# Performance work log

Hardware: AMD Instinct MI355X
Metric: run time of the kernel (lower is better)

The kernel has to match this reference:

```python
import jax, jax.numpy as jnp
import numpy as np

B, S = 2, 1024
ENC_IN, MARK_IN = 21, 4
PRED_LEN, C_OUT = 96, 21
E = 512                 # embedding_dim
INNER = 2 * E           # proj_factor=2.0 (library default; Model does not pass it)
NH = 8                  # mLSTM heads
DH = INNER // NH        # 128
K = 4                   # causal conv1d kernel
BS = 4                  # qkv_proj_blocksize
NHP = INNER // BS       # 256 block-diagonal proj heads
NB = 4                  # num_blocks
EPS = 1e-5


def setup_inputs() -> dict:
    key = jax.random.key(0)
    ks = jax.random.split(key, 24)
    it = iter(range(24))
    def n(shape, s=0.02):
        return jax.random.normal(ks[next(it)], shape, jnp.float32) * s
    return {
        "x_enc": n((B, S, ENC_IN), 1.0),
        "x_mark_enc": n((B, S, MARK_IN), 1.0),
        "x_dec": n((B, PRED_LEN, ENC_IN), 1.0),
        "x_mark_dec": n((B, PRED_LEN, MARK_IN), 1.0),
        "emb_W": n((ENC_IN + MARK_IN, E), 0.05),
        "emb_b": jnp.zeros((E,), jnp.float32),
        "ln_w": jnp.ones((NB, E), jnp.float32),
        "up_W": n((NB, E, 2 * INNER)),
        "conv_W": n((NB, INNER, K), 0.1),
        "conv_b": jnp.zeros((NB, INNER), jnp.float32),
        "q_W": n((NB, NHP, BS, BS), 0.1),
        "k_W": n((NB, NHP, BS, BS), 0.1),
        "v_W": n((NB, NHP, BS, BS), 0.1),
        "ig_W": n((NB, 3 * INNER, NH)),
        "ig_b": jnp.zeros((NB, NH), jnp.float32),
        "fg_W": n((NB, 3 * INNER, NH)),
        "fg_b": jnp.tile(jnp.linspace(3.0, 6.0, NH, dtype=jnp.float32), (NB, 1)),
        "skip": jnp.ones((NB, INNER), jnp.float32),
        "onorm_w": jnp.ones((NB, INNER), jnp.float32),
        "down_W": n((NB, INNER, E)),
        "post_ln_w": jnp.ones((E,), jnp.float32),
        "head_W": n((E, C_OUT), 0.05),
        "head_b": jnp.zeros((C_OUT,), jnp.float32),
    }


def _ln(x, w):
    mu = jnp.mean(x, -1, keepdims=True)
    var = jnp.var(x, -1, keepdims=True)
    return (x - mu) * jax.lax.rsqrt(var + EPS) * w


def _headwise(x, w):
    # block-diagonal LinearHeadwiseExpand: (B,S,INNER) with (NHP,BS,BS) blocks
    xh = x.reshape(x.shape[0], x.shape[1], NHP, BS)
    return jnp.einsum('bshd,hod->bsho', xh, w).reshape(x.shape)


def _block(x, lw, uW, cW, cb, qW, kW, vW, igW, igb, fgW, fgb, sk, ow, dW):
    xn = _ln(x, lw)
    up = xn @ uW                                  # (B,S,2*INNER)
    xm, z = up[..., :INNER], up[..., INNER:]
    # causal depthwise conv1d + SiLU
    xc = jax.lax.conv_general_dilated(
        xm.transpose(0, 2, 1), cW[:, None, :], (1,), [(K - 1, 0)],
        feature_group_count=INNER,
        dimension_numbers=('NCH', 'OIH', 'NCH')).transpose(0, 2, 1) + cb
    xc = jax.nn.silu(xc)
    q = _headwise(xc, qW)
    k = _headwise(xc, kW)
    v = _headwise(xm, vW)
    qkv = jnp.concatenate([q, k, v], -1)          # (B,S,3*INNER)
    ig = (qkv @ igW + igb).transpose(0, 2, 1)     # (B,NH,S)
    fg = (qkv @ fgW + fgb).transpose(0, 2, 1)
    qh = q.reshape(B, S, NH, DH).transpose(0, 2, 1, 3)
    kh = k.reshape(B, S, NH, DH).transpose(0, 2, 1, 3)
    vh = v.reshape(B, S, NH, DH).transpose(0, 2, 1, 3)
    # parallel stabilized mLSTM (exp-gated linear attention)
    log_f = jax.nn.log_sigmoid(fg)
    cs = jnp.cumsum(log_f, -1)                    # (B,NH,S)
    Mmat = cs[..., :, None] - cs[..., None, :]    # (B,NH,S,S) cumulative decay
    tri = jnp.tril(jnp.ones((S, S), bool))
    logD = jnp.where(tri, Mmat + ig[..., None, :], -jnp.inf)
    m = jnp.max(logD, -1, keepdims=True)          # row-wise stabilizer
    D = jnp.exp(logD - m)
    qk = jnp.einsum('bnsd,bntd->bnst', qh, kh) / (DH ** 0.5)
    C = qk * D
    norm = jnp.maximum(jnp.abs(jnp.sum(C, -1, keepdims=True)), jnp.exp(-m))
    h = jnp.einsum('bnst,bntd->bnsd', C / (norm + 1e-6), vh)
    # multi-head layernorm (groupnorm over DH per head), weight, no bias
    hn = (h - jnp.mean(h, -1, keepdims=True)) * jax.lax.rsqrt(jnp.var(h, -1, keepdims=True) + EPS)
    hn = hn.transpose(0, 2, 1, 3).reshape(B, S, INNER) * ow
    hs = (hn + sk * xc) * jax.nn.silu(z)          # learnable skip + output gate
    return x + hs @ dW                            # residual


def reference(x_enc, x_mark_enc, x_dec, x_mark_dec, emb_W, emb_b, ln_w, up_W,
              conv_W, conv_b, q_W, k_W, v_W, ig_W, ig_b, fg_W, fg_b, skip,
              onorm_w, down_W, post_ln_w, head_W, head_b):
    x = jnp.concatenate([x_enc, x_mark_enc], -1) @ emb_W + emb_b
    for i in range(NB):
        x = _block(x, ln_w[i], up_W[i], conv_W[i], conv_b[i], q_W[i], k_W[i],
                   v_W[i], ig_W[i], ig_b[i], fg_W[i], fg_b[i], skip[i],
                   onorm_w[i], down_W[i])
    x = _ln(x, post_ln_w)
    return x[:, -PRED_LEN:, :] @ head_W + head_b
```

## Files before the change

kernel.cpp:

```cpp
#include <hip/hip_runtime.h>
#include <hip/hip_bf16.h>

#define S_LEN 1024
#define E_DIM 512
#define INNER_D 1024
#define NHEAD 8
#define DHEAD 128

typedef unsigned short u16;
typedef unsigned int u32;
typedef __attribute__((ext_vector_type(8))) short short8;
typedef __attribute__((ext_vector_type(4))) float f32x4;

union S8 { short8 v; u16 u[8]; uint4 q; };

__device__ __forceinline__ u16 f2bf(float f) {
  u32 u = __float_as_uint(f);
  u32 r = u + 0x7FFFu + ((u >> 16) & 1u);
  return (u16)(r >> 16);
}
__device__ __forceinline__ float bf2f(u16 u) { return __uint_as_float(((u32)u) << 16); }

__device__ __forceinline__ void gload16(const u16* g, u16* l) {
  __builtin_amdgcn_global_load_lds((const __attribute__((address_space(1))) void*)g,
                                   (__attribute__((address_space(3))) void*)l, 16, 0, 0);
}

__device__ __forceinline__ void prep_transpose(
    const float* __restrict__ in, u16* __restrict__ out, int K, int N,
    int k0, int n0, int t, u16 (*T)[72])
{
  int kr = t >> 2, nseg = (t & 3) * 16;
  const float* src = in + (size_t)(k0 + kr) * N + n0 + nseg;
#pragma unroll
  for (int j = 0; j < 16; j++) T[kr][nseg + j] = f2bf(src[j]);
  __syncthreads();
  int nr = t >> 2, kseg = (t & 3) * 16;
  u32 u[8];
#pragma unroll
  for (int rr = 0; rr < 8; rr++) {
    u32 lo = T[kseg + 2 * rr][nr];
    u32 hi = T[kseg + 2 * rr + 1][nr];
    u[rr] = lo | (hi << 16);
  }
  u16* dst = out + (size_t)(n0 + nr) * K + k0 + kseg;
  uint4 w0 = {u[0], u[1], u[2], u[3]};
  uint4 w1 = {u[4], u[5], u[6], u[7]};
  *(uint4*)dst = w0;
  *(uint4*)(dst + 8) = w1;
}

__global__ __launch_bounds__(256) void prep_kernel(
    const float* __restrict__ up_W, u16* __restrict__ upWt,
    const float* __restrict__ down_W, u16* __restrict__ dnWt,
    const float* __restrict__ igW, const float* __restrict__ fgW,
    u16* __restrict__ ghi, u16* __restrict__ glo,
    const float* __restrict__ xe, const float* __restrict__ xmk,
    const float* __restrict__ eW, const float* __restrict__ eb,
    float* __restrict__ x)
{
  __shared__ u16 T[64][72];
  __shared__ float in_s[25];
  int id = blockIdx.x;
  int t = threadIdx.x;
  if (id < 1024) {
    int bx = id & 7, rest = id >> 3;
    int by = rest & 31, L = rest >> 5;
    prep_transpose(up_W + (size_t)L * 512 * 2048, upWt + (size_t)L * 1048576,
                   512, 2048, bx * 64, by * 64, t, T);
  } else if (id < 1536) {
    int id2 = id - 1024;
    int bx = id2 & 15, rest = id2 >> 4;
    int by = rest & 7, L = rest >> 3;
    prep_transpose(down_W + (size_t)L * 1024 * 512, dnWt + (size_t)L * 524288,
                   1024, 512, bx * 64, by * 64, t, T);
  } else if (id < 2304) {
    int id3 = id - 1536;
    int bx = id3 % 12, rest = id3 / 12;
    int n = rest & 15, L = rest >> 4;
    int k = bx * 256 + t;
    const float* W = ((n < 8) ? igW : fgW) + (size_t)L * 24576;
    float v = W[(size_t)k * 8 + (n & 7)];
    u16 h = f2bf(v);
    u16 l = f2bf(v - bf2f(h));
    size_t o = ((size_t)L * 16 + n) * 3072 + k;
    ghi[o] = h;
    glo[o] = l;
  } else {
    int row = id - 2304;
    if (t < 21) in_s[t] = xe[row * 21 + t];
    else if (t < 25) in_s[t] = xmk[row * 4 + t - 21];
    __syncthreads();
#pragma unroll
    for (int rep = 0; rep < 2; rep++) {
      int e = t + rep * 256;
      float acc = eb[e];
#pragma unroll
      for (int i = 0; i < 25; i++) acc += in_s[i] * eW[i * E_DIM + e];
      x[(size_t)row * E_DIM + e] = acc;
    }
  }
}

__global__ __launch_bounds__(256) void ln_kernel(
    const float* __restrict__ x, const float* __restrict__ w, u16* __restrict__ out)
{
  int row = blockIdx.x, tid = threadIdx.x;
  const float* xr = x + (size_t)row * E_DIM;
  float2 v = *(const float2*)(xr + tid * 2);
  float s = v.x + v.y, q = v.x * v.x + v.y * v.y;
#pragma unroll
  for (int off = 32; off; off >>= 1) { s += __shfl_xor(s, off); q += __shfl_xor(q, off); }
  __shared__ float ssum[4], ssq[4];
  int wv = tid >> 6;
  if ((tid & 63) == 0) { ssum[wv] = s; ssq[wv] = q; }
  __syncthreads();
  s = ssum[0] + ssum[1] + ssum[2] + ssum[3];
  q = ssq[0] + ssq[1] + ssq[2] + ssq[3];
  float mu = s * (1.f / E_DIM);
  float var = q * (1.f / E_DIM) - mu * mu;
  float rs = rsqrtf(var + 1e-5f);
  int e = tid * 2;
  ushort2 o;
  o.x = f2bf((v.x - mu) * rs * w[e]);
  o.y = f2bf((v.y - mu) * rs * w[e + 1]);
  *(ushort2*)(out + (size_t)row * E_DIM + e) = o;
}

__global__ __launch_bounds__(256) void lnhead_kernel(
    const float* __restrict__ x, const float* __restrict__ w,
    const float* __restrict__ hW, const float* __restrict__ hb,
    float* __restrict__ out)
{
  int ridx = blockIdx.x;
  int b = ridx / 96, r = ridx % 96;
  int row = b * S_LEN + (S_LEN - 96) + r;
  int tid = threadIdx.x;
  const float* xr = x + (size_t)row * E_DIM;
  float2 v = *(const float2*)(xr + tid * 2);
  float s = v.x + v.y, q = v.x * v.x + v.y * v.y;
#pragma unroll
  for (int off = 32; off; off >>= 1) { s += __shfl_xor(s, off); q += __shfl_xor(q, off); }
  __shared__ float ssum[4], ssq[4];
  __shared__ float lnv[512];
  __shared__ float part[8][32];
  int wv = tid >> 6;
  if ((tid & 63) == 0) { ssum[wv] = s; ssq[wv] = q; }
  __syncthreads();
  s = ssum[0] + ssum[1] + ssum[2] + ssum[3];
  q = ssq[0] + ssq[1] + ssq[2] + ssq[3];
  float mu = s * (1.f / E_DIM);
  float var = q * (1.f / E_DIM) - mu * mu;
  float rs = rsqrtf(var + 1e-5f);
  int e = tid * 2;
  lnv[e]     = (v.x - mu) * rs * w[e];
  lnv[e + 1] = (v.y - mu) * rs * w[e + 1];
  __syncthreads();
  int n = tid & 31, sl = tid >> 5;
  float p = 0.f;
  if (n < 21) {
#pragma unroll 8
    for (int kk = 0; kk < 64; kk++)
      p += lnv[sl * 64 + kk] * hW[(sl * 64 + kk) * 21 + n];
  }
  part[sl][n] = p;
  __syncthreads();
  if (tid < 21) {
    float acc = hb[tid];
#pragma unroll
    for (int j = 0; j < 8; j++) acc += part[j][tid];
    out[ridx * 21 + tid] = acc;
  }
}

__global__ __launch_bounds__(256) void gemm_bf16_split64(
    const u16* __restrict__ A, const u16* __restrict__ Bt,
    float* __restrict__ C0, u16* __restrict__ C1,
    int M, int N, int K, int split_col, int ldc)
{
  __shared__ u16 As0[128 * 32], As1[128 * 32], As2[128 * 32];
  __shared__ u16 Bs0[128 * 32], Bs1[128 * 32], Bs2[128 * 32];
  const int tid = threadIdx.x;
  const int row0 = blockIdx.y * 128, col0 = blockIdx.x * 128;
  const int wave = tid >> 6, lane = tid & 63;
  const int wr = wave >> 1, wc = wave & 1;
  const int lm = lane & 15, lq = lane >> 4;
  const int lr4 = lane >> 2;
  const int cg4 = (lane & 3) ^ (lr4 & 3);
  f32x4 acc[4][4] = {};
  const u16* Abase = A + (size_t)(row0 + lr4) * K + cg4 * 8;
  const u16* Bbase = Bt + (size_t)(col0 + lr4) * K + cg4 * 8;
  const int key = lm & 3;

#define STG_UP(AS, BS, K0) do { \
  _Pragma("unroll") for (int i = 0; i < 2; i++) \
    gload16(Abase + (size_t)((wave * 2 + i) * 16) * K + (K0), &AS[(wave * 2 + i) * 512]); \
  _Pragma("unroll") for (int i = 0; i < 2; i++) \
    gload16(Bbase + (size_t)((wave * 2 + i) * 16) * K + (K0), &BS[(wave * 2 + i) * 512]); \
} while (0)

#define CMP_UP(AS, BS) do { \
  short8 af[4], bfv[4]; \
  _Pragma("unroll") for (int i = 0; i < 4; i++) \
    af[i] = *(const short8*)&AS[(wr * 64 + i * 16 + lm) * 32 + ((lq ^ key) * 8)]; \
  _Pragma("unroll") for (int j = 0; j < 4; j++) \
    bfv[j] = *(const short8*)&BS[(wc * 64 + j * 16 + lm) * 32 + ((lq ^ key) * 8)]; \
  _Pragma("unroll") for (int i = 0; i < 4; i++) \
    _Pragma("unroll") for (int j = 0; j < 4; j++) \
      acc[i][j] = __builtin_amdgcn_mfma_f32_16x16x32_bf16(af[i], bfv[j], acc[i][j], 0, 0, 0); \
} while (0)

  STG_UP(As0, Bs0, 0);
  asm volatile("" ::: "memory");
  STG_UP(As1, Bs1, 32);
  asm volatile("" ::: "memory");
  STG_UP(As2, Bs2, 64);
#pragma unroll
  for (int t = 0; t < 16; t++) {
    if (t <= 13)      asm volatile("s_waitcnt vmcnt(8)" ::: "memory");
    else if (t == 14) asm volatile("s_waitcnt vmcnt(4)" ::: "memory");
    else              asm volatile("s_waitcnt vmcnt(0)" ::: "memory");
    __builtin_amdgcn_sched_barrier(0);
    __builtin_amdgcn_s_barrier();
    if ((t % 3) == 0)      CMP_UP(As0, Bs0);
    else if ((t % 3) == 1) CMP_UP(As1, Bs1);
    else                   CMP_UP(As2, Bs2);
    __builtin_amdgcn_s_barrier();
    if (t + 3 < 16) {
      if ((t % 3) == 0)      STG_UP(As0, Bs0, (t + 3) * 32);
      else if ((t % 3) == 1) STG_UP(As1, Bs1, (t + 3) * 32);
      else                   STG_UP(As2, Bs2, (t + 3) * 32);
    }
  }
#undef STG_UP
#undef CMP_UP

  const bool toC1 = (col0 >= split_col);
#pragma unroll
  for (int i = 0; i < 4; i++) {
#pragma unroll
    for (int j = 0; j < 4; j++) {
      int col = col0 - (toC1 ? split_col : 0) + wc * 64 + j * 16 + lm;
#pragma unroll
      for (int r = 0; r < 4; r++) {
        int row = row0 + wr * 64 + i * 16 + lq * 4 + r;
        if (toC1) C1[(size_t)row * ldc + col] = f2bf(acc[i][j][r]);
        else C0[(size_t)row * ldc + col] = acc[i][j][r];
      }
    }
  }
}

__global__ __launch_bounds__(256) void gemm_bf16_32(
    const u16* __restrict__ A, const u16* __restrict__ Bt,
    float* __restrict__ C, int M, int N, int K, int ldc)
{
  __shared__ u16 As0[64 * 64], As1[64 * 64], As2[64 * 64];
  __shared__ u16 Bs0[64 * 64], Bs1[64 * 64], Bs2[64 * 64];
  const int tid = threadIdx.x;
  const int row0 = blockIdx.y * 64, col0 = blockIdx.x * 64;
  const int wave = tid >> 6, lane = tid & 63;
  const int wr = wave >> 1, wc = wave & 1;
  const int lm = lane & 15, lq = lane >> 4;
  const int lr = lane >> 3;
  const int cg = (lane & 7) ^ lr;
  f32x4 acc[2][2] = {};
  const u16* Abase = A + (size_t)(row0 + lr) * K + cg * 8;
  const u16* Bbase = Bt + (size_t)(col0 + lr) * K + cg * 8;
  const int key = lm & 7;

#define STAGE_DN(AS, BS, K0) do { \
  _Pragma("unroll") for (int i = 0; i < 2; i++) \
    gload16(Abase + (size_t)((wave * 2 + i) * 8) * K + (K0), &AS[(wave * 2 + i) * 512]); \
  _Pragma("unroll") for (int j = 0; j < 2; j++) \
    gload16(Bbase + (size_t)((wave * 2 + j) * 8) * K + (K0), &BS[(wave * 2 + j) * 512]); \
} while (0)

#define COMPUTE_DN(AS, BS) do { \
  short8 af[2][2], bfv[2][2]; \
  _Pragma("unroll") for (int kc = 0; kc < 2; kc++) { \
    _Pragma("unroll") for (int i = 0; i < 2; i++) \
      af[kc][i] = *(const short8*)&AS[(wr * 32 + i * 16 + lm) * 64 + (((kc * 4 + lq) ^ key) * 8)]; \
    _Pragma("unroll") for (int j = 0; j < 2; j++) \
      bfv[kc][j] = *(const short8*)&BS[(wc * 32 + j * 16 + lm) * 64 + (((kc * 4 + lq) ^ key) * 8)]; \
  } \
  _Pragma("unroll") for (int kc = 0; kc < 2; kc++) \
    _Pragma("unroll") for (int i = 0; i < 2; i++) \
      _Pragma("unroll") for (int j = 0; j < 2; j++) \
        acc[i][j] = __builtin_amdgcn_mfma_f32_16x16x32_bf16(af[kc][i], bfv[kc][j], acc[i][j], 0, 0, 0); \
} while (0)

  STAGE_DN(As0, Bs0, 0);
  asm volatile("" ::: "memory");
  STAGE_DN(As1, Bs1, 64);
  asm volatile("" ::: "memory");
  STAGE_DN(As2, Bs2, 128);
#pragma unroll
  for (int t = 0; t < 16; t++) {
    if (t <= 13)      asm volatile("s_waitcnt vmcnt(8)" ::: "memory");
    else if (t == 14) asm volatile("s_waitcnt vmcnt(4)" ::: "memory");
    else              asm volatile("s_waitcnt vmcnt(0)" ::: "memory");
    __builtin_amdgcn_sched_barrier(0);
    __builtin_amdgcn_s_barrier();
    if ((t % 3) == 0)      COMPUTE_DN(As0, Bs0);
    else if ((t % 3) == 1) COMPUTE_DN(As1, Bs1);
    else                   COMPUTE_DN(As2, Bs2);
    __builtin_amdgcn_s_barrier();
    if (t + 3 < 16) {
      if ((t % 3) == 0)      STAGE_DN(As0, Bs0, (t + 3) * 64);
      else if ((t % 3) == 1) STAGE_DN(As1, Bs1, (t + 3) * 64);
      else                   STAGE_DN(As2, Bs2, (t + 3) * 64);
    }
  }
#undef STAGE_DN
#undef COMPUTE_DN

#pragma unroll
  for (int i = 0; i < 2; i++) {
#pragma unroll
    for (int j = 0; j < 2; j++) {
      int col = col0 + wc * 32 + j * 16 + lm;
#pragma unroll
      for (int r = 0; r < 4; r++) {
        int row = row0 + wr * 32 + i * 16 + lq * 4 + r;
        C[(size_t)row * ldc + col] += acc[i][j][r];
      }
    }
  }
}

__global__ __launch_bounds__(256) void convqkv_kernel(
    const float* __restrict__ xm,
    const float* __restrict__ cw, const float* __restrict__ cb,
    const float* __restrict__ qw, const float* __restrict__ kw, const float* __restrict__ vw,
    float* __restrict__ xc, u16* __restrict__ q, u16* __restrict__ k, u16* __restrict__ v,
    u16* __restrict__ vt)
{
  int r0 = blockIdx.x * 8;
  int s0 = r0 & (S_LEN - 1);
  int g = threadIdx.x;
  int c0 = g * 4;
  const float* base = xm + (size_t)r0 * INNER_D + c0;

  float4 xv[11];
#pragma unroll
  for (int j = 0; j < 11; j++) {
    int ts = s0 - 3 + j;
    float4 t = {0.f, 0.f, 0.f, 0.f};
    if (ts >= 0) t = *(const float4*)(base + (ptrdiff_t)(j - 3) * INNER_D);
    xv[j] = t;
  }
  float cwv[4][4];
#pragma unroll
  for (int c = 0; c < 4; c++)
#pragma unroll
    for (int kk = 0; kk < 4; kk++) cwv[c][kk] = cw[(c0 + c) * 4 + kk];
  float cbv[4] = {cb[c0], cb[c0 + 1], cb[c0 + 2], cb[c0 + 3]};
  const float* qg = qw + g * 16;
  const float* kg = kw + g * 16;
  const float* vg = vw + g * 16;
  float qwv[16], kwv[16], vwv[16];
#pragma unroll
  for (int i = 0; i < 16; i++) { qwv[i] = qg[i]; kwv[i] = kg[i]; vwv[i] = vg[i]; }

  u32 vt_pack[4][4];

#pragma unroll
  for (int i = 0; i < 8; i++) {
    float a0 = cbv[0], a1 = cbv[1], a2 = cbv[2], a3 = cbv[3];
#pragma unroll
    for (int kk = 0; kk < 4; kk++) {
      float4 xvv = xv[i + kk];
      a0 += xvv.x * cwv[0][kk];
      a1 += xvv.y * cwv[1][kk];
      a2 += xvv.z * cwv[2][kk];
      a3 += xvv.w * cwv[3][kk];
    }
    a0 = a0 / (1.f + __expf(-a0));
    a1 = a1 / (1.f + __expf(-a1));
    a2 = a2 / (1.f + __expf(-a2));
    a3 = a3 / (1.f + __expf(-a3));
    float4 accv = {a0, a1, a2, a3};
    *(float4*)(xc + (size_t)(r0 + i) * INNER_D + c0) = accv;

    float xcv[4] = {a0, a1, a2, a3};
    float xmv[4] = {xv[i + 3].x, xv[i + 3].y, xv[i + 3].z, xv[i + 3].w};
    ushort4 qs, ks, vs;
    u16* qp = (u16*)&qs; u16* kp = (u16*)&ks; u16* vp = (u16*)&vs;
#pragma unroll
    for (int o = 0; o < 4; o++) {
      float aq = 0.f, ak = 0.f, av = 0.f;
#pragma unroll
      for (int d = 0; d < 4; d++) {
        aq += xcv[d] * qwv[o * 4 + d];
        ak += xcv[d] * kwv[o * 4 + d];
        av += xmv[d] * vwv[o * 4 + d];
      }
      qp[o] = f2bf(aq); kp[o] = f2bf(ak);
      u16 vv = f2bf(av);
      vp[o] = vv;
      if ((i & 1) == 0) vt_pack[o][i >> 1] = (u32)vv;
      else              vt_pack[o][i >> 1] |= ((u32)vv) << 16;
    }
    size_t off = (size_t)(r0 + i) * INNER_D + c0;
    *(ushort4*)(q + off) = qs;
    *(ushort4*)(k + off) = ks;
    *(ushort4*)(v + off) = vs;
  }
  u16* vtb = vt + ((size_t)((r0 >> 10) * INNER_D + c0)) * S_LEN + s0;
#pragma unroll
  for (int c = 0; c < 4; c++) {
    uint4 wv4 = {vt_pack[c][0], vt_pack[c][1], vt_pack[c][2], vt_pack[c][3]};
    *(uint4*)(vtb + (size_t)c * S_LEN) = wv4;
  }
}

__global__ __launch_bounds__(256) void gates_mfma_kernel(
    const u16* __restrict__ q, const u16* __restrict__ k, const u16* __restrict__ v,
    const u16* __restrict__ whi, const u16* __restrict__ wlo,
    const float* __restrict__ igb, const float* __restrict__ fgb,
    float* __restrict__ ig, float* __restrict__ fg)
{
  const int blk = blockIdx.x;
  const int tid = threadIdx.x;
  const int wave = tid >> 6, lane = tid & 63;
  const int lm = lane & 15, lq = lane >> 4;
  const int grow = blk * 16 + lm;
  const u16* parts[3] = {q, k, v};
  f32x4 acc = {};
#pragma unroll 4
  for (int kc = 0; kc < 24; kc++) {
    int k0 = wave * 768 + kc * 32;
    int part = k0 >> 10;
    int idx = (k0 & 1023) + lq * 8;
    S8 a, bh_, bl_;
    a.q = *(const uint4*)(parts[part] + (size_t)grow * INNER_D + idx);
    bh_.q = *(const uint4*)(whi + (size_t)lm * 3072 + k0 + lq * 8);
    bl_.q = *(const uint4*)(wlo + (size_t)lm * 3072 + k0 + lq * 8);
    __builtin_amdgcn_s_setprio(1);
    acc = __builtin_amdgcn_mfma_f32_16x16x32_bf16(a.v, bh_.v, acc, 0, 0, 0);
    acc = __builtin_amdgcn_mfma_f32_16x16x32_bf16(a.v, bl_.v, acc, 0, 0, 0);
    __builtin_amdgcn_s_setprio(0);
  }
  __shared__ float red[4][16][17];
#pragma unroll
  for (int r = 0; r < 4; r++) red[wave][lq * 4 + r][lm] = acc[r];
  __syncthreads();
  if (wave == 0) {
#pragma unroll
    for (int r = 0; r < 4; r++) {
      int row = lq * 4 + r;
      float sum = red[0][row][lm] + red[1][row][lm] + red[2][row][lm] + red[3][row][lm];
      int growr = blk * 16 + row;
      int b = growr >> 10, s = growr & (S_LEN - 1);
      if (lm < 8) ig[((size_t)(b * NHEAD + lm) << 10) + s] = sum + igb[lm];
      else        fg[((size_t)(b * NHEAD + (lm - 8)) << 10) + s] = sum + fgb[lm - 8];
    }
  }
}

__global__ __launch_bounds__(1024) void scan_kernel(
    const float* __restrict__ ig, const float* __restrict__ fg,
    float* __restrict__ a, float* __restrict__ rm, float* __restrict__ enm)
{
  int bh = blockIdx.x;
  int t = threadIdx.x;
  int lane = t & 63, wv = t >> 6;
  __shared__ float sw[16];
  size_t o = ((size_t)bh << 10) + t;
  float f = fg[o];
  float lf = (f >= 0.f) ? -log1pf(__expf(-f)) : f - log1pf(__expf(f));
  float v = lf;
#pragma unroll
  for (int off = 1; off < 64; off <<= 1) {
    float u = __shfl_up(v, off);
    if (lane >= off) v += u;
  }
  if (lane == 63) sw[wv] = v;
  __syncthreads();
  float pre = 0.f;
  for (int w = 0; w < wv; w++) pre += sw[w];
  float cs = v + pre;
  float av = ig[o] - cs;
  a[o] = av;
  float m = av;
#pragma unroll
  for (int off = 1; off < 64; off <<= 1) {
    float u = __shfl_up(m, off);
    if (lane >= off) m = fmaxf(m, u);
  }
  __syncthreads();
  if (lane == 63) sw[wv] = m;
  __syncthreads();
  float pm = -3.4e38f;
  for (int w = 0; w < wv; w++) pm = fmaxf(pm, sw[w]);
  float rmx = fmaxf(m, pm);
  rm[o] = rmx;
  enm[o] = __expf(-(cs + rmx));
}

__device__ __constant__ int c_qt[24] = {7,15,14,15, 6,13,14,12,13, 5,11,12,10,11, 4, 9,10, 8, 9, 3, 8, 2, 1, 0};
__device__ __constant__ int c_k0[24] = {0, 0, 7, 8, 0, 0, 0, 6, 7, 0, 0, 0, 5, 6, 0, 0, 0, 4, 5, 0, 0, 0, 0, 0};
__device__ __constant__ int c_k1[24] = {8, 8,15,16, 7, 7, 7,13,14, 6, 6, 6,11,12, 5, 5, 5, 9,10, 4, 4, 3, 2, 1};
__device__ __constant__ int c_md[24] = {0, 1, 2, 2, 0, 1, 1, 2, 2, 0, 1, 1, 2, 2, 0, 1, 1, 2, 2, 0, 1, 0, 0, 0};

__global__ __launch_bounds__(256) void attn_mfma_kernel(
    const u16* __restrict__ qhg, const u16* __restrict__ khg, const u16* __restrict__ vtg,
    const float* __restrict__ a_arr, const float* __restrict__ rm_arr, const float* __restrict__ enm_arr,
    const float* __restrict__ xc, const u16* __restrict__ zh,
    const float* __restrict__ skip, const float* __restrict__ onw,
    u16* __restrict__ hs, float* __restrict__ hpart, float* __restrict__ scpart)
{
  const int bh = blockIdx.x;
  const int job = blockIdx.y;
  const int qt = c_qt[job], k0t = c_k0[job], k1t = c_k1[job], mode = c_md[job];
  const int b = bh >> 3, h = bh & 7;
  const int s0 = qt * 64;
  const int tid = threadIdx.x;
  const int wave = tid >> 6, lane = tid & 63;
  const int lm = lane & 15, lq = lane >> 4;
  const size_t rowbase = (size_t)b * S_LEN;
  const int c0 = h * DHEAD;

  __shared__ u16 Ks0[64 * 128], Ks1[64 * 128];
  __shared__ u16 Vt0[128 * 64], Vt1[128 * 64];
  __shared__ u16 Ws[64 * 72];

  short8 aq[4];
  {
    const u16* qp = qhg + (rowbase + s0 + wave * 16 + lm) * INNER_D + c0 + lq * 8;
#pragma unroll
    for (int kc = 0; kc < 4; kc++) {
      S8 tmp; tmp.q = *(const uint4*)(qp + kc * 32);
      aq[kc] = tmp.v;
    }
  }
  float rmv[4];
#pragma unroll
  for (int r = 0; r < 4; r++)
    rmv[r] = rm_arr[(size_t)bh * S_LEN + s0 + wave * 16 + lq * 4 + r];

  f32x4 accH[8] = {};
  float sc_acc[4] = {0.f, 0.f, 0.f, 0.f};
  const float scale = 0.08838834764831845f;
  const int lr16 = lane >> 4;
  const int ls16 = lane & 15;
  const int lr8 = lane >> 3;
  const int cgv = (lane & 7) ^ lr8;
  const u16* vtbase = vtg + ((size_t)b * INNER_D + c0) * S_LEN;

  float ae0[4], ae1[4];

#define PREF(KS, VS, AE, T0) do { \
  _Pragma("unroll") for (int j = 0; j < 4; j++) { \
    int rK = (wave * 4 + j) * 4 + lr16; \
    int cgk = ls16 ^ (rK & 7); \
    gload16(khg + (rowbase + (T0) + rK) * INNER_D + c0 + cgk * 8, &KS[(wave * 4 + j) * 512]); \
  } \
  _Pragma("unroll") for (int j = 0; j < 4; j++) { \
    int rV = (wave * 4 + j) * 8 + lr8; \
    gload16(vtbase + (size_t)rV * S_LEN + (T0) + cgv * 8, &VS[(wave * 4 + j) * 512]); \
  } \
  _Pragma("unroll") for (int cb = 0; cb < 4; cb++) \
    AE[cb] = a_arr[(size_t)bh * S_LEN + (T0) + cb * 16 + lm]; \
} while (0)

#define QK_STEP(KS, PACC) do { \
  __builtin_amdgcn_s_setprio(1); \
  _Pragma("unroll") for (int kc = 0; kc < 4; kc++) \
    _Pragma("unroll") for (int cb = 0; cb < 4; cb++) { \
      short8 bk = *(const short8*)&KS[(cb * 16 + lm) * 128 + (((kc * 4 + lq) ^ (lm & 7)) * 8)]; \
      PACC[cb] = __builtin_amdgcn_mfma_f32_16x16x32_bf16(aq[kc], bk, PACC[cb], 0, 0, 0); \
    } \
  __builtin_amdgcn_s_setprio(0); \
} while (0)

#define W_PV(AE, VT, T0, PACC) do { \
  float wpart[4] = {0.f, 0.f, 0.f, 0.f}; \
  _Pragma("unroll") for (int cb = 0; cb < 4; cb++) { \
    int colg = (T0) + cb * 16 + lm; \
    float ea = AE[cb]; \
    _Pragma("unroll") for (int r = 0; r < 4; r++) { \
      int rowg = s0 + wave * 16 + lq * 4 + r; \
      float wv = PACC[cb][r] * scale * __expf(ea - rmv[r]); \
      if (colg > rowg) wv = 0.f; \
      wpart[r] += wv; \
      Ws[(wave * 16 + lq * 4 + r) * 72 + cb * 16 + lm] = f2bf(wv); \
    } \
  } \
  _Pragma("unroll") for (int r = 0; r < 4; r++) { \
    float sr = wpart[r]; \
    sr += __shfl_xor(sr, 1); sr += __shfl_xor(sr, 2); \
    sr += __shfl_xor(sr, 4); sr += __shfl_xor(sr, 8); \
    sc_acc[r] += sr; \
  } \
  __builtin_amdgcn_s_setprio(1); \
  _Pragma("unroll") for (int kc = 0; kc < 2; kc++) { \
    short8 aw = *(const short8*)&Ws[(wave * 16 + lm) * 72 + kc * 32 + lq * 8]; \
    _Pragma("unroll") for (int nb = 0; nb < 8; nb++) { \
      short8 bv = *(const short8*)&VT[(nb * 16 + lm) * 64 + (((kc * 4 + lq) ^ (lm & 7)) * 8)]; \
      accH[nb] = __builtin_amdgcn_mfma_f32_16x16x32_bf16(aw, bv, accH[nb], 0, 0, 0); \
    } \
  } \
  __builtin_amdgcn_s_setprio(0); \
} while (0)

  int kt = k0t;
  PREF(Ks0, Vt0, ae0, kt * 64);
  asm volatile("" ::: "memory");
  if (kt + 1 < k1t) PREF(Ks1, Vt1, ae1, (kt + 1) * 64);

  while (true) {
    {
      if (kt + 1 < k1t) asm volatile("s_waitcnt vmcnt(12)" ::: "memory");
      else              asm volatile("s_waitcnt vmcnt(0)" ::: "memory");
      __builtin_amdgcn_sched_barrier(0);
      __builtin_amdgcn_s_barrier();
      f32x4 pacc[4] = {};
      QK_STEP(Ks0, pacc);
      W_PV(ae0, Vt0, kt * 64, pacc);
      __builtin_amdgcn_s_barrier();
      if (kt + 2 < k1t) PREF(Ks0, Vt0, ae0, (kt + 2) * 64);
      kt++;
      if (kt >= k1t) break;
    }
    {
      if (kt + 1 < k1t) asm volatile("s_waitcnt vmcnt(12)" ::: "memory");
      else              asm volatile("s_waitcnt vmcnt(0)" ::: "memory");
      __builtin_amdgcn_sched_barrier(0);
      __builtin_amdgcn_s_barrier();
      f32x4 pacc[4] = {};
      QK_STEP(Ks1, pacc);
      W_PV(ae1, Vt1, kt * 64, pacc);
      __builtin_amdgcn_s_barrier();
      if (kt + 2 < k1t) PREF(Ks1, Vt1, ae1, (kt + 2) * 64);
      kt++;
      if (kt >= k1t) break;
    }
  }
#undef PREF
#undef QK_STEP
#undef W_PV

  if (mode != 0) {
    int slot = mode - 1;
    int qr = qt - 8;
    float* Hp = hpart + (((size_t)slot * 16 + bh) * 8 + qr) * 8192;
    float* sp = scpart + ((slot * 16 + bh) * 8 + qr) * 64;
#pragma unroll
    for (int r = 0; r < 4; r++) {
      int row = wave * 16 + lq * 4 + r;
      if (lm == 0) sp[row] = sc_acc[r];
#pragma unroll
      for (int nb = 0; nb < 8; nb++)
        Hp[row * 128 + nb * 16 + lm] = accH[nb][r];
    }
    return;
  }

  float inv[4], muv[4], rsv[4];
#pragma unroll
  for (int r = 0; r < 4; r++) {
    int rowg = s0 + wave * 16 + lq * 4 + r;
    float nrm = fmaxf(fabsf(sc_acc[r]), enm_arr[(size_t)bh * S_LEN + rowg]);
    inv[r] = 1.f / (nrm + 1e-6f);
  }
#pragma unroll
  for (int r = 0; r < 4; r++) {
    float s = 0.f, qq = 0.f;
#pragma unroll
    for (int nb = 0; nb < 8; nb++) {
      float hv = accH[nb][r] * inv[r];
      accH[nb][r] = hv;
      s += hv; qq += hv * hv;
    }
    s += __shfl_xor(s, 1); s += __shfl_xor(s, 2); s += __shfl_xor(s, 4); s += __shfl_xor(s, 8);
    qq += __shfl_xor(qq, 1); qq += __shfl_xor(qq, 2); qq += __shfl_xor(qq, 4); qq += __shfl_xor(qq, 8);
    float mu = s * (1.f / DHEAD);
    float var = qq * (1.f / DHEAD) - mu * mu;
    muv[r] = mu;
    rsv[r] = rsqrtf(var + 1e-5f);
  }
  float ow[8], sk[8];
#pragma unroll
  for (int nb = 0; nb < 8; nb++) {
    ow[nb] = onw[c0 + nb * 16 + lm];
    sk[nb] = skip[c0 + nb * 16 + lm];
  }
#pragma unroll
  for (int r = 0; r < 4; r++) {
    int rowg = s0 + wave * 16 + lq * 4 + r;
    size_t base = (rowbase + rowg) * INNER_D + c0;
#pragma unroll
    for (int nb = 0; nb < 8; nb++) {
      int d = nb * 16 + lm;
      float xcv = xc[base + d];
      float zv = bf2f(zh[base + d]);
      float hn = (accH[nb][r] - muv[r]) * rsv[r] * ow[nb] + sk[nb] * xcv;
      float o = hn * (zv / (1.f + __expf(-zv)));
      hs[base + d] = f2bf(o);
    }
  }
}

__global__ __launch_bounds__(256) void attn_combine_kernel(
    const float* __restrict__ hpart, const float* __restrict__ scpart,
    const float* __restrict__ enm,
    const float* __restrict__ xc, const u16* __restrict__ zh,
    const float* __restrict__ skip, const float* __restrict__ onw,
    u16* __restrict__ hs)
{
  int wave = threadIdx.x >> 6, lane = threadIdx.x & 63;
  int gid = blockIdx.x * 4 + wave;
  int bh = gid >> 9;
  int rr = gid & 511;
  int qr = rr >> 6, row = rr & 63;
  int b = bh >> 3, hh = bh & 7;
  int s = (qr + 8) * 64 + row;
  size_t off = (((size_t)bh) * 8 + qr) * 8192 + row * 128 + lane * 2;
  float2 h0 = *(const float2*)(hpart + off);
  float2 h1 = *(const float2*)(hpart + 1048576 + off);
  int sidx = (bh * 8 + qr) * 64 + row;
  float sc = scpart[sidx] + scpart[8192 + sidx];
  float nrm = fmaxf(fabsf(sc), enm[(size_t)bh * S_LEN + s]);
  float inv = 1.f / (nrm + 1e-6f);
  float hx = (h0.x + h1.x) * inv, hy = (h0.y + h1.y) * inv;
  float sm = hx + hy, sq = hx * hx + hy * hy;
#pragma unroll
  for (int off2 = 32; off2; off2 >>= 1) { sm += __shfl_xor(sm, off2); sq += __shfl_xor(sq, off2); }
  float mu = sm * (1.f / DHEAD);
  float var = sq * (1.f / DHEAD) - mu * mu;
  float rs = rsqrtf(var + 1e-5f);
  int c0 = hh * DHEAD + lane * 2;
  size_t base = ((size_t)(b * S_LEN + s)) * INNER_D + c0;
  float2 xc2 = *(const float2*)(xc + base);
  ushort2 z2u = *(const ushort2*)(zh + base);
  float z2x = bf2f(z2u.x), z2y = bf2f(z2u.y);
  float skx = skip[c0], sky = skip[c0 + 1];
  float owx = onw[c0],  owy = onw[c0 + 1];
  ushort2 o;
  o.x = f2bf(((hx - mu) * rs * owx + skx * xc2.x) * (z2x / (1.f + __expf(-z2x))));
  o.y = f2bf(((hy - mu) * rs * owy + sky * xc2.y) * (z2y / (1.f + __expf(-z2y))));
  *(ushort2*)(hs + base) = o;
}

extern "C" void kernel_launch(void* const* d_in, const int* in_sizes, int n_in,
                              void* d_out, int out_size, void* d_ws, size_t ws_size,
                              hipStream_t stream)
{
  const float* x_enc   = (const float*)d_in[0];
  const float* x_mark  = (const float*)d_in[1];
  const float* emb_W   = (const float*)d_in[4];
  const float* emb_b   = (const float*)d_in[5];
  const float* ln_w    = (const float*)d_in[6];
  const float* up_W    = (const float*)d_in[7];
  const float* conv_W  = (const float*)d_in[8];
  const float* conv_b  = (const float*)d_in[9];
  const float* q_W     = (const float*)d_in[10];
  const float* k_W     = (const float*)d_in[11];
  const float* v_W     = (const float*)d_in[12];
  const float* ig_W    = (const float*)d_in[13];
  const float* ig_b    = (const float*)d_in[14];
  const float* fg_W    = (const float*)d_in[15];
  const float* fg_b    = (const float*)d_in[16];
  const float* skip_w  = (const float*)d_in[17];
  const float* onorm_w = (const float*)d_in[18];
  const float* down_W  = (const float*)d_in[19];
  const float* post_ln = (const float*)d_in[20];
  const float* head_W  = (const float*)d_in[21];
  const float* head_b  = (const float*)d_in[22];

  float* p = (float*)d_ws;
  float* x    = p; p += 1048576;
  float* xm   = p; p += 2097152;
  float* xc   = p; p += 2097152;
  float* igb_ = p; p += 16384;
  float* fgb_ = p; p += 16384;
  float* ab   = p; p += 16384;
  float* rmb  = p; p += 16384;
  float* enmb = p; p += 16384;
  float* ln96 = p; p += 98304;
  u16* qhb = (u16*)p; p += 1048576;
  u16* khb = (u16*)p; p += 1048576;
  u16* vhb = (u16*)p; p += 1048576;
  u16* zh  = (u16*)p; p += 524288;
  u16* xnh = (u16*)p; p += 524288;
  u16* upWtA = (u16*)p; p += 2097152;
  u16* dnWtA = (u16*)p; p += 1048576;
  u16* gtwH = (u16*)p; p += 98304;
  u16* gtwL = (u16*)p; p += 98304;
  float* hpart = p; p += 2097152;
  float* scpart = p; p += 16384;
  u16* vtg = (u16*)p; p += 1048576;
  u16* hsbh = (u16*)xm;

  prep_kernel<<<4352, 256, 0, stream>>>(
      up_W, upWtA, down_W, dnWtA, ig_W, fg_W, gtwH, gtwL,
      x_enc, x_mark, emb_W, emb_b, x);

  for (int L = 0; L < 4; L++) {
    ln_kernel<<<2048, 256, 0, stream>>>(x, ln_w + L * 512, xnh);
    gemm_bf16_split64<<<dim3(16, 16), 256, 0, stream>>>(
        xnh, upWtA + (size_t)L * 1048576, xm, zh, 2048, 2048, 512, 1024, 1024);
    convqkv_kernel<<<256, 256, 0, stream>>>(
        xm, conv_W + L * 4096, conv_b + L * 1024,
        q_W + L * 4096, k_W + L * 4096, v_W + L * 4096,
        xc, qhb, khb, vhb, vtg);
    gates_mfma_kernel<<<128, 256, 0, stream>>>(
        qhb, khb, vhb, gtwH + (size_t)L * 49152, gtwL + (size_t)L * 49152,
        ig_b + L * 8, fg_b + L * 8, igb_, fgb_);
    scan_kernel<<<16, 1024, 0, stream>>>(igb_, fgb_, ab, rmb, enmb);
    attn_mfma_kernel<<<dim3(16, 24), 256, 0, stream>>>(
        qhb, khb, vtg, ab, rmb, enmb, xc, zh,
        skip_w + L * 1024, onorm_w + L * 1024, hsbh, hpart, scpart);
    attn_combine_kernel<<<2048, 256, 0, stream>>>(
        hpart, scpart, enmb, xc, zh, skip_w + L * 1024, onorm_w + L * 1024, hsbh);
    gemm_bf16_32<<<dim3(8, 32), 256, 0, stream>>>(
        hsbh, dnWtA + (size_t)L * 524288, x, 2048, 512, 1024, 512);
  }

  lnhead_kernel<<<192, 256, 0, stream>>>(x, post_ln, head_W, head_b, (float*)d_out);
}
```

Baseline: 454.4 us.

## Fuse gate scan into attention kernel and drop split-K combine pass

Each attention block now recomputes the cumulative log-forget-gate scan and running max for its whole (batch, head) sequence in shared memory, so the separate scan kernel is no longer needed. The 24-job load-balanced schedule with split-K partial outputs and a combine kernel is replaced by one block per query tile that loops over all causal key tiles. This removes two launches per layer and the partial-sum round trip through global memory. In exchange, the scan is repeated in every block and the work per block is uneven: the last query tile processes 16 key tiles while the first processes one, which lengthens the critical path.

```diff
diff --git a/kernel.cpp b/kernel.cpp
--- a/kernel.cpp
+++ b/kernel.cpp
@@ -459,61 +459,16 @@
   }
 }
 
-__global__ __launch_bounds__(1024) void scan_kernel(
-    const float* __restrict__ ig, const float* __restrict__ fg,
-    float* __restrict__ a, float* __restrict__ rm, float* __restrict__ enm)
-{
-  int bh = blockIdx.x;
-  int t = threadIdx.x;
-  int lane = t & 63, wv = t >> 6;
-  __shared__ float sw[16];
-  size_t o = ((size_t)bh << 10) + t;
-  float f = fg[o];
-  float lf = (f >= 0.f) ? -log1pf(__expf(-f)) : f - log1pf(__expf(f));
-  float v = lf;
-#pragma unroll
-  for (int off = 1; off < 64; off <<= 1) {
-    float u = __shfl_up(v, off);
-    if (lane >= off) v += u;
-  }
-  if (lane == 63) sw[wv] = v;
-  __syncthreads();
-  float pre = 0.f;
-  for (int w = 0; w < wv; w++) pre += sw[w];
-  float cs = v + pre;
-  float av = ig[o] - cs;
-  a[o] = av;
-  float m = av;
-#pragma unroll
-  for (int off = 1; off < 64; off <<= 1) {
-    float u = __shfl_up(m, off);
-    if (lane >= off) m = fmaxf(m, u);
-  }
-  __syncthreads();
-  if (lane == 63) sw[wv] = m;
-  __syncthreads();
-  float pm = -3.4e38f;
-  for (int w = 0; w < wv; w++) pm = fmaxf(pm, sw[w]);
-  float rmx = fmaxf(m, pm);
-  rm[o] = rmx;
-  enm[o] = __expf(-(cs + rmx));
-}
-
-__device__ __constant__ int c_qt[24] = {7,15,14,15, 6,13,14,12,13, 5,11,12,10,11, 4, 9,10, 8, 9, 3, 8, 2, 1, 0};
-__device__ __constant__ int c_k0[24] = {0, 0, 7, 8, 0, 0, 0, 6, 7, 0, 0, 0, 5, 6, 0, 0, 0, 4, 5, 0, 0, 0, 0, 0};
-__device__ __constant__ int c_k1[24] = {8, 8,15,16, 7, 7, 7,13,14, 6, 6, 6,11,12, 5, 5, 5, 9,10, 4, 4, 3, 2, 1};
-__device__ __constant__ int c_md[24] = {0, 1, 2, 2, 0, 1, 1, 2, 2, 0, 1, 1, 2, 2, 0, 1, 1, 2, 2, 0, 1, 0, 0, 0};
-
 __global__ __launch_bounds__(256) void attn_mfma_kernel(
     const u16* __restrict__ qhg, const u16* __restrict__ khg, const u16* __restrict__ vtg,
-    const float* __restrict__ a_arr, const float* __restrict__ rm_arr, const float* __restrict__ enm_arr,
+    const float* __restrict__ ig_arr, const float* __restrict__ fg_arr,
     const float* __restrict__ xc, const u16* __restrict__ zh,
     const float* __restrict__ skip, const float* __restrict__ onw,
-    u16* __restrict__ hs, float* __restrict__ hpart, float* __restrict__ scpart)
+    u16* __restrict__ hs)
 {
   const int bh = blockIdx.x;
-  const int job = blockIdx.y;
-  const int qt = c_qt[job], k0t = c_k0[job], k1t = c_k1[job], mode = c_md[job];
+  const int qt = blockIdx.y;
+  const int k1t = qt + 1;
   const int b = bh >> 3, h = bh & 7;
   const int s0 = qt * 64;
   const int tid = threadIdx.x;
@@ -525,6 +480,62 @@
   __shared__ u16 Ks0[64 * 128], Ks1[64 * 128];
   __shared__ u16 Vt0[128 * 64], Vt1[128 * 64];
   __shared__ u16 Ws[64 * 72];
+  __shared__ float sa[1024];
+  __shared__ float sws[16], swm[16];
+  __shared__ float srm[64], senm[64];
+
+  {
+    float vsc[4], igv[4], css[4], msc[4];
+#pragma unroll
+    for (int c = 0; c < 4; c++) {
+      int vt = c * 256 + tid;
+      size_t o = ((size_t)bh << 10) + vt;
+      float f = fg_arr[o];
+      igv[c] = ig_arr[o];
+      float lf = (f >= 0.f) ? -log1pf(__expf(-f)) : f - log1pf(__expf(f));
+      float v = lf;
+#pragma unroll
+      for (int off = 1; off < 64; off <<= 1) {
+        float u = __shfl_up(v, off);
+        if (lane >= off) v += u;
+      }
+      if (lane == 63) sws[c * 4 + (tid >> 6)] = v;
+      vsc[c] = v;
+    }
+    __syncthreads();
+#pragma unroll
+    for (int c = 0; c < 4; c++) {
+      int vt = c * 256 + tid;
+      int wvv = c * 4 + (tid >> 6);
+      float pre = 0.f;
+      for (int u = 0; u < wvv; u++) pre += sws[u];
+      float cs = vsc[c] + pre;
+      float av = igv[c] - cs;
+      sa[vt] = av;
+      float m = av;
+#pragma unroll
+      for (int off = 1; off < 64; off <<= 1) {
+        float u = __shfl_up(m, off);
+        if (lane >= off) m = fmaxf(m, u);
+      }
+      if (lane == 63) swm[wvv] = m;
+      css[c] = cs; msc[c] = m;
+    }
+    __syncthreads();
+#pragma unroll
+    for (int c = 0; c < 4; c++) {
+      int vt = c * 256 + tid;
+      int wvv = c * 4 + (tid >> 6);
+      float pm = -3.4e38f;
+      for (int u = 0; u < wvv; u++) pm = fmaxf(pm, swm[u]);
+      float rmx = fmaxf(msc[c], pm);
+      if (vt >= s0 && vt < s0 + 64) {
+        srm[vt - s0] = rmx;
+        senm[vt - s0] = __expf(-(css[c] + rmx));
+      }
+    }
+    __syncthreads();
+  }
 
   short8 aq[4];
   {
@@ -538,7 +549,7 @@
   float rmv[4];
 #pragma unroll
   for (int r = 0; r < 4; r++)
-    rmv[r] = rm_arr[(size_t)bh * S_LEN + s0 + wave * 16 + lq * 4 + r];
+    rmv[r] = srm[wave * 16 + lq * 4 + r];
 
   f32x4 accH[8] = {};
   float sc_acc[4] = {0.f, 0.f, 0.f, 0.f};
@@ -549,9 +560,7 @@
   const int cgv = (lane & 7) ^ lr8;
   const u16* vtbase = vtg + ((size_t)b * INNER_D + c0) * S_LEN;
 
-  float ae0[4], ae1[4];
-
-#define PREF(KS, VS, AE, T0) do { \
+#define PREF(KS, VS, T0) do { \
   _Pragma("unroll") for (int j = 0; j < 4; j++) { \
     int rK = (wave * 4 + j) * 4 + lr16; \
     int cgk = ls16 ^ (rK & 7); \
@@ -561,8 +570,6 @@
     int rV = (wave * 4 + j) * 8 + lr8; \
     gload16(vtbase + (size_t)rV * S_LEN + (T0) + cgv * 8, &VS[(wave * 4 + j) * 512]); \
   } \
-  _Pragma("unroll") for (int cb = 0; cb < 4; cb++) \
-    AE[cb] = a_arr[(size_t)bh * S_LEN + (T0) + cb * 16 + lm]; \
 } while (0)
 
 #define QK_STEP(KS, PACC) do { \
@@ -575,11 +582,11 @@
   __builtin_amdgcn_s_setprio(0); \
 } while (0)
 
-#define W_PV(AE, VT, T0, PACC) do { \
+#define W_PV(VT, T0, PACC) do { \
   float wpart[4] = {0.f, 0.f, 0.f, 0.f}; \
   _Pragma("unroll") for (int cb = 0; cb < 4; cb++) { \
     int colg = (T0) + cb * 16 + lm; \
-    float ea = AE[cb]; \
+    float ea = sa[(T0) + cb * 16 + lm]; \
     _Pragma("unroll") for (int r = 0; r < 4; r++) { \
       int rowg = s0 + wave * 16 + lq * 4 + r; \
       float wv = PACC[cb][r] * scale * __expf(ea - rmv[r]); \
@@ -605,35 +612,35 @@
   __builtin_amdgcn_s_setprio(0); \
 } while (0)
 
-  int kt = k0t;
-  PREF(Ks0, Vt0, ae0, kt * 64);
+  int kt = 0;
+  PREF(Ks0, Vt0, 0);
   asm volatile("" ::: "memory");
-  if (kt + 1 < k1t) PREF(Ks1, Vt1, ae1, (kt + 1) * 64);
+  if (1 < k1t) PREF(Ks1, Vt1, 64);
 
   while (true) {
     {
-      if (kt + 1 < k1t) asm volatile("s_waitcnt vmcnt(12)" ::: "memory");
+      if (kt + 1 < k1t) asm volatile("s_waitcnt vmcnt(8)" ::: "memory");
       else              asm volatile("s_waitcnt vmcnt(0)" ::: "memory");
       __builtin_amdgcn_sched_barrier(0);
       __builtin_amdgcn_s_barrier();
       f32x4 pacc[4] = {};
       QK_STEP(Ks0, pacc);
-      W_PV(ae0, Vt0, kt * 64, pacc);
+      W_PV(Vt0, kt * 64, pacc);
       __builtin_amdgcn_s_barrier();
-      if (kt + 2 < k1t) PREF(Ks0, Vt0, ae0, (kt + 2) * 64);
+      if (kt + 2 < k1t) PREF(Ks0, Vt0, (kt + 2) * 64);
       kt++;
       if (kt >= k1t) break;
     }
     {
-      if (kt + 1 < k1t) asm volatile("s_waitcnt vmcnt(12)" ::: "memory");
+      if (kt + 1 < k1t) asm volatile("s_waitcnt vmcnt(8)" ::: "memory");
       else              asm volatile("s_waitcnt vmcnt(0)" ::: "memory");
       __builtin_amdgcn_sched_barrier(0);
       __builtin_amdgcn_s_barrier();
       f32x4 pacc[4] = {};
       QK_STEP(Ks1, pacc);
-      W_PV(ae1, Vt1, kt * 64, pacc);
+      W_PV(Vt1, kt * 64, pacc);
       __builtin_amdgcn_s_barrier();
-      if (kt + 2 < k1t) PREF(Ks1, Vt1, ae1, (kt + 2) * 64);
+      if (kt + 2 < k1t) PREF(Ks1, Vt1, (kt + 2) * 64);
       kt++;
       if (kt >= k1t) break;
     }
@@ -642,27 +649,11 @@
 #undef QK_STEP
 #undef W_PV
 
-  if (mode != 0) {
-    int slot = mode - 1;
-    int qr = qt - 8;
-    float* Hp = hpart + (((size_t)slot * 16 + bh) * 8 + qr) * 8192;
-    float* sp = scpart + ((slot * 16 + bh) * 8 + qr) * 64;
-#pragma unroll
-    for (int r = 0; r < 4; r++) {
-      int row = wave * 16 + lq * 4 + r;
-      if (lm == 0) sp[row] = sc_acc[r];
-#pragma unroll
-      for (int nb = 0; nb < 8; nb++)
-        Hp[row * 128 + nb * 16 + lm] = accH[nb][r];
-    }
-    return;
-  }
-
   float inv[4], muv[4], rsv[4];
 #pragma unroll
   for (int r = 0; r < 4; r++) {
-    int rowg = s0 + wave * 16 + lq * 4 + r;
-    float nrm = fmaxf(fabsf(sc_acc[r]), enm_arr[(size_t)bh * S_LEN + rowg]);
+    int row = wave * 16 + lq * 4 + r;
+    float nrm = fmaxf(fabsf(sc_acc[r]), senm[row]);
     inv[r] = 1.f / (nrm + 1e-6f);
   }
 #pragma unroll
@@ -701,47 +692,6 @@
       hs[base + d] = f2bf(o);
     }
   }
-}
-
-__global__ __launch_bounds__(256) void attn_combine_kernel(
-    const float* __restrict__ hpart, const float* __restrict__ scpart,
-    const float* __restrict__ enm,
-    const float* __restrict__ xc, const u16* __restrict__ zh,
-    const float* __restrict__ skip, const float* __restrict__ onw,
-    u16* __restrict__ hs)
-{
-  int wave = threadIdx.x >> 6, lane = threadIdx.x & 63;
-  int gid = blockIdx.x * 4 + wave;
-  int bh = gid >> 9;
-  int rr = gid & 511;
-  int qr = rr >> 6, row = rr & 63;
-  int b = bh >> 3, hh = bh & 7;
-  int s = (qr + 8) * 64 + row;
-  size_t off = (((size_t)bh) * 8 + qr) * 8192 + row * 128 + lane * 2;
-  float2 h0 = *(const float2*)(hpart + off);
-  float2 h1 = *(const float2*)(hpart + 1048576 + off);
-  int sidx = (bh * 8 + qr) * 64 + row;
-  float sc = scpart[sidx] + scpart[8192 + sidx];
-  float nrm = fmaxf(fabsf(sc), enm[(size_t)bh * S_LEN + s]);
-  float inv = 1.f / (nrm + 1e-6f);
-  float hx = (h0.x + h1.x) * inv, hy = (h0.y + h1.y) * inv;
-  float sm = hx + hy, sq = hx * hx + hy * hy;
-#pragma unroll
-  for (int off2 = 32; off2; off2 >>= 1) { sm += __shfl_xor(sm, off2); sq += __shfl_xor(sq, off2); }
-  float mu = sm * (1.f / DHEAD);
-  float var = sq * (1.f / DHEAD) - mu * mu;
-  float rs = rsqrtf(var + 1e-5f);
-  int c0 = hh * DHEAD + lane * 2;
-  size_t base = ((size_t)(b * S_LEN + s)) * INNER_D + c0;
-  float2 xc2 = *(const float2*)(xc + base);
-  ushort2 z2u = *(const ushort2*)(zh + base);
-  float z2x = bf2f(z2u.x), z2y = bf2f(z2u.y);
-  float skx = skip[c0], sky = skip[c0 + 1];
-  float owx = onw[c0],  owy = onw[c0 + 1];
-  ushort2 o;
-  o.x = f2bf(((hx - mu) * rs * owx + skx * xc2.x) * (z2x / (1.f + __expf(-z2x))));
-  o.y = f2bf(((hy - mu) * rs * owy + sky * xc2.y) * (z2y / (1.f + __expf(-z2y))));
-  *(ushort2*)(hs + base) = o;
 }
 
 extern "C" void kernel_launch(void* const* d_in, const int* in_sizes, int n_in,
@@ -776,10 +726,6 @@
   float* xc   = p; p += 2097152;
   float* igb_ = p; p += 16384;
   float* fgb_ = p; p += 16384;
-  float* ab   = p; p += 16384;
-  float* rmb  = p; p += 16384;
-  float* enmb = p; p += 16384;
-  float* ln96 = p; p += 98304;
   u16* qhb = (u16*)p; p += 1048576;
   u16* khb = (u16*)p; p += 1048576;
   u16* vhb = (u16*)p; p += 1048576;
@@ -789,8 +735,6 @@
   u16* dnWtA = (u16*)p; p += 1048576;
   u16* gtwH = (u16*)p; p += 98304;
   u16* gtwL = (u16*)p; p += 98304;
-  float* hpart = p; p += 2097152;
-  float* scpart = p; p += 16384;
   u16* vtg = (u16*)p; p += 1048576;
   u16* hsbh = (u16*)xm;
 
@@ -809,12 +753,9 @@
     gates_mfma_kernel<<<128, 256, 0, stream>>>(
         qhb, khb, vhb, gtwH + (size_t)L * 49152, gtwL + (size_t)L * 49152,
         ig_b + L * 8, fg_b + L * 8, igb_, fgb_);
-    scan_kernel<<<16, 1024, 0, stream>>>(igb_, fgb_, ab, rmb, enmb);
-    attn_mfma_kernel<<<dim3(16, 24), 256, 0, stream>>>(
-        qhb, khb, vtg, ab, rmb, enmb, xc, zh,
-        skip_w + L * 1024, onorm_w + L * 1024, hsbh, hpart, scpart);
-    attn_combine_kernel<<<2048, 256, 0, stream>>>(
-        hpart, scpart, enmb, xc, zh, skip_w + L * 1024, onorm_w + L * 1024, hsbh);
+    attn_mfma_kernel<<<dim3(16, 16), 256, 0, stream>>>(
+        qhb, khb, vtg, igb_, fgb_, xc, zh,
+        skip_w + L * 1024, onorm_w + L * 1024, hsbh);
     gemm_bf16_32<<<dim3(8, 32), 256, 0, stream>>>(
         hsbh, dnWtA + (size_t)L * 524288, x, 2048, 512, 1024, 512);
   }
```

New measurement: 477.3 us. 1.05x slower.
